# Kernel optimization log

Hardware: AMD Instinct MI355X
Metric: run time of the kernel (lower is better)

## Reference

```python
import jax, jax.numpy as jnp
import numpy as np

N = 50000      # nodes
E = 1_600_000  # edges (avg degree 32)
D = 128        # in/hidden channels
OUT = 64       # out channels


def setup_inputs() -> dict:
    key = jax.random.key(0)
    ks = jax.random.split(key, 12)
    s = 0.08  # ~glorot scale for 128-dim
    return {
        "x": jax.random.normal(ks[0], (N, D), jnp.float32),
        "edge_index": jax.random.randint(ks[1], (2, E), 0, N, dtype=jnp.int64),
        # GCN layer 1
        "W1": jax.random.normal(ks[2], (D, D), jnp.float32) * s,
        "b1": jnp.zeros((D,), jnp.float32),
        # GraphSAGE layer 2 (mean aggregation): lin_l on neighbors, lin_r on root
        "Wl": jax.random.normal(ks[3], (D, D), jnp.float32) * s,
        "Wr": jax.random.normal(ks[4], (D, D), jnp.float32) * s,
        "bs": jnp.zeros((D,), jnp.float32),
        # GAT layer 3 (heads=1, concat=False)
        "Wg": jax.random.normal(ks[5], (D, D), jnp.float32) * s,
        "a_s": jax.random.normal(ks[6], (D,), jnp.float32) * s,
        "a_d": jax.random.normal(ks[7], (D,), jnp.float32) * s,
        "bg": jnp.zeros((D,), jnp.float32),
        # GCN output layer
        "Wo": jax.random.normal(ks[8], (D, OUT), jnp.float32) * s,
        "bo": jnp.zeros((OUT,), jnp.float32),
    }


def _self_loops(src, dst, n):
    loop = jnp.arange(n, dtype=src.dtype)
    return jnp.concatenate([src, loop]), jnp.concatenate([dst, loop])


def gcn_conv(x, W, b, src, dst, n):
    # PyG GCNConv: add self-loops, symmetric normalization D^-1/2 (A+I) D^-1/2
    s2, d2 = _self_loops(src, dst, n)
    deg = jax.ops.segment_sum(jnp.ones_like(d2, dtype=x.dtype), d2, num_segments=n)
    dinv = jnp.where(deg > 0, jax.lax.rsqrt(deg), 0.0)
    h = x @ W                         # [n, out]
    norm = dinv[s2] * dinv[d2]        # [E+n]
    out = jax.ops.segment_sum(h[s2] * norm[:, None], d2, num_segments=n)
    return out + b


def sage_conv(x, Wl, Wr, b, src, dst, n):
    # PyG SAGEConv, aggr='mean': W_l * mean_neigh + W_r * x (no self-loops)
    deg = jax.ops.segment_sum(jnp.ones_like(dst, dtype=x.dtype), dst, num_segments=n)
    agg = jax.ops.segment_sum(x[src], dst, num_segments=n)
    mean = agg / jnp.maximum(deg, 1.0)[:, None]
    return mean @ Wl + x @ Wr + b


def gat_conv(x, W, a_s, a_d, b, src, dst, n):
    # PyG GATConv heads=1, concat=False: self-loops, edge softmax over incoming edges
    h = x @ W                               # [n, out]
    s2, d2 = _self_loops(src, dst, n)
    alpha_src = h @ a_s                     # [n]
    alpha_dst = h @ a_d                     # [n]
    e = jax.nn.leaky_relu(alpha_src[s2] + alpha_dst[d2], negative_slope=0.2)
    m = jax.ops.segment_max(e, d2, num_segments=n)   # every node has a self-loop
    ex = jnp.exp(e - m[d2])
    denom = jax.ops.segment_sum(ex, d2, num_segments=n)
    alpha = ex / denom[d2]
    out = jax.ops.segment_sum(alpha[:, None] * h[s2], d2, num_segments=n)
    return out + b


def reference(x, edge_index, W1, b1, Wl, Wr, bs, Wg, a_s, a_d, bg, Wo, bo):
    src, dst = edge_index[0], edge_index[1]
    n = x.shape[0]
    # eval mode: F.dropout(training=False) is identity
    h = jax.nn.relu(gcn_conv(x, W1, b1, src, dst, n))
    h = jax.nn.relu(sage_conv(h, Wl, Wr, bs, src, dst, n))
    h = jax.nn.relu(gat_conv(h, Wg, a_s, a_d, bg, src, dst, n))
    return gcn_conv(h, Wo, bo, src, dst, n)
```

## Files before the change

kernel.cpp:

```cpp
#include <hip/hip_runtime.h>
#include <math.h>


#define BUCKET_BITS 8
#define BUCKET_SZ   256
#define NBMAX       256
#define CAP         10240

typedef short short8 __attribute__((ext_vector_type(8)));
typedef float f32x4 __attribute__((ext_vector_type(4)));
typedef float f32x2 __attribute__((ext_vector_type(2)));
typedef unsigned int u32x4 __attribute__((ext_vector_type(4)));
typedef unsigned short u16x8 __attribute__((ext_vector_type(8)));
typedef int int4a __attribute__((ext_vector_type(4), aligned(4)));
typedef float float4a __attribute__((ext_vector_type(4), aligned(4)));

__device__ __forceinline__ float leaky02(float x) { return x > 0.0f ? x : 0.2f * x; }
__device__ __forceinline__ float bflo(unsigned u) { return __uint_as_float(u << 16); }
__device__ __forceinline__ float bfhi(unsigned u) { return __uint_as_float(u & 0xFFFF0000u); }
__device__ __forceinline__ unsigned short f2bf(float f) {
    unsigned u = __float_as_uint(f);
    u += 0x7FFFu + ((u >> 16) & 1u);
    return (unsigned short)(u >> 16);
}

template<int NO, bool AFP32, bool SCALE, bool BIASRELU, bool DUAL, bool DOTS>
__global__ __launch_bounds__(256) void mgemm_k(
    const void* __restrict__ Av, const float* __restrict__ W,
    const void* __restrict__ A1v, const float* __restrict__ W1,
    unsigned short* __restrict__ C16,
    const float* __restrict__ scale, const float* __restrict__ bias,
    const float* __restrict__ a_s, const float* __restrict__ a_d,
    float* __restrict__ as_, float* __restrict__ ad_, int n)
{
    constexpr int CT = NO / 16;
    __shared__ unsigned short Wp[128 * NO];
    const int tid = threadIdx.x;
    const int wave = tid >> 6, lane = tid & 63;
    const int q = lane >> 4, ml = lane & 15;
    const int row0 = blockIdx.x * 64 + wave * 16;
    int arow = row0 + ml; if (arow >= n) arow = n - 1;

    f32x4 acc[CT];
#pragma unroll
    for (int c = 0; c < CT; c++) acc[c] = {0.f, 0.f, 0.f, 0.f};

    for (int half = 0; half < (DUAL ? 2 : 1); half++) {
        const float* Wsrc = half ? W1 : W;
        const void* Asrc = half ? A1v : Av;
        __syncthreads();
        for (int f = tid; f < 64 * (NO / 4); f += 256) {
            const int kp = f / (NO / 4);
            const int n4 = f % (NO / 4);
            const float4 a = *(const float4*)(Wsrc + (size_t)(2 * kp) * NO + n4 * 4);
            const float4 b = *(const float4*)(Wsrc + (size_t)(2 * kp + 1) * NO + n4 * 4);
            const int k = 2 * kp, kb = k >> 5, qq = (k >> 3) & 3, p = (k & 7) >> 1;
            const float av[4] = {a.x, a.y, a.z, a.w};
            const float bv[4] = {b.x, b.y, b.z, b.w};
#pragma unroll
            for (int j = 0; j < 4; j++) {
                int col = n4 * 4 + j;
                int c = col >> 4, nl = col & 15;
                unsigned pk = (unsigned)f2bf(av[j]) | ((unsigned)f2bf(bv[j]) << 16);
                ((unsigned*)Wp)[(((kb * CT + c) * 64) + qq * 16 + nl) * 4 + p] = pk;
            }
        }
        __syncthreads();
#pragma unroll
        for (int kb = 0; kb < 4; kb++) {
            short8 afr;
            if (AFP32) {
                const float* Af = (const float*)Asrc + (size_t)arow * 128 + kb * 32 + q * 8;
#pragma unroll
                for (int j = 0; j < 8; j++) afr[j] = (short)f2bf(Af[j]);
            } else {
                afr = *(const short8*)((const unsigned short*)Asrc +
                                       ((size_t)kb * n + arow) * 32 + q * 8);
            }
#pragma unroll
            for (int c = 0; c < CT; c++) {
                short8 bfr = *(const short8*)(Wp + ((size_t)(kb * CT + c) * 64 + lane) * 8);
                acc[c] = __builtin_amdgcn_mfma_f32_16x16x32_bf16(afr, bfr, acc[c], 0, 0, 0);
            }
        }
    }

    if (DOTS) {
        float ps[4] = {0.f, 0.f, 0.f, 0.f}, pd[4] = {0.f, 0.f, 0.f, 0.f};
#pragma unroll
        for (int c = 0; c < CT; c++) {
            float sv = a_s[c * 16 + ml], dv = a_d[c * 16 + ml];
#pragma unroll
            for (int r = 0; r < 4; r++) {
                ps[r] = fmaf(acc[c][r], sv, ps[r]);
                pd[r] = fmaf(acc[c][r], dv, pd[r]);
            }
        }
#pragma unroll
        for (int off = 1; off < 16; off <<= 1) {
#pragma unroll
            for (int r = 0; r < 4; r++) {
                ps[r] += __shfl_xor(ps[r], off, 64);
                pd[r] += __shfl_xor(pd[r], off, 64);
            }
        }
        if (ml == 0) {
#pragma unroll
            for (int r = 0; r < 4; r++) {
                int row = row0 + q * 4 + r;
                if (row < n) { as_[row] = ps[r]; ad_[row] = pd[r]; }
            }
        }
    }

    float sc[4];
    if (SCALE) {
#pragma unroll
        for (int r = 0; r < 4; r++) {
            int row = row0 + q * 4 + r;
            sc[r] = scale[row < n ? row : 0];
        }
    }
#pragma unroll
    for (int c = 0; c < CT; c++) {
        float bv = BIASRELU ? bias[c * 16 + ml] : 0.0f;
        const int col = c * 16 + ml;
#pragma unroll
        for (int r = 0; r < 4; r++) {
            int row = row0 + q * 4 + r;
            if (row < n) {
                float v = acc[c][r];
                if (SCALE) v *= sc[r];
                if (BIASRELU) v = fmaxf(v + bv, 0.0f);
                C16[((size_t)(col >> 5) * n + row) * 32 + (col & 31)] = f2bf(v);
            }
        }
    }
}

__global__ void binit_k(int* __restrict__ bcur, int nb) {
    int t = threadIdx.x;
    if (t < nb) bcur[t] = t * CAP;
}

#define PART_CH 4096
__global__ __launch_bounds__(256) void part_k(
    const int* __restrict__ src, const int* __restrict__ dst,
    int* __restrict__ bcur, unsigned long long* __restrict__ part, int nE)
{
    __shared__ int cnt[NBMAX];
    __shared__ int cur[NBMAX];
    const int base = blockIdx.x * PART_CH;
    const int t = threadIdx.x;
    cnt[t] = 0;
    __syncthreads();
    int d[PART_CH / 256], s[PART_CH / 256];
#pragma unroll
    for (int j = 0; j < PART_CH / 256; j++) {
        int e = base + j * 256 + t;
        if (e < nE) {
            d[j] = dst[e]; s[j] = src[e];
            atomicAdd(&cnt[d[j] >> BUCKET_BITS], 1);
        } else d[j] = -1;
    }
    __syncthreads();
    {
        int c = cnt[t];
        cur[t] = c ? atomicAdd(&bcur[t], c) : 0;
    }
    __syncthreads();
#pragma unroll
    for (int j = 0; j < PART_CH / 256; j++) {
        if (d[j] >= 0) {
            int p = atomicAdd(&cur[d[j] >> BUCKET_BITS], 1);
            part[p] = ((unsigned long long)(unsigned)d[j] << 32) | (unsigned)s[j];
        }
    }
}

__global__ __launch_bounds__(256) void bscan_k(const int* __restrict__ bcur,
                                               int* __restrict__ bofs, int nb) {
    __shared__ int sm[256];
    const int t = threadIdx.x;
    int v = (t < nb) ? (bcur[t] - t * CAP) : 0;
    sm[t] = v;
    __syncthreads();
    for (int off = 1; off < 256; off <<= 1) {
        int tv = (t >= off) ? sm[t - off] : 0;
        __syncthreads();
        sm[t] += tv;
        __syncthreads();
    }
    if (t < nb) {
        bofs[t] = sm[t] - v;
        if (t == nb - 1) bofs[nb] = sm[t];
    }
}

__global__ __launch_bounds__(256) void csr_k(
    const unsigned long long* __restrict__ part, const int* __restrict__ bcur,
    const int* __restrict__ bofs, int* __restrict__ rowptr, int* __restrict__ srcs,
    float* __restrict__ dinv, float* __restrict__ invm, int n, int nE)
{
    __shared__ int lcnt[BUCKET_SZ];
    __shared__ int sm[BUCKET_SZ];
    __shared__ int lcur[BUCKET_SZ];
    const int b = blockIdx.x;
    const int t = threadIdx.x;
    const int base_in = b * CAP;
    const int cntE = bcur[b] - base_in;
    const int base_out = bofs[b];

    lcnt[t] = 0;
    __syncthreads();
#pragma unroll 4
    for (int e = t; e < cntE; e += 256) {
        int dl = (int)(part[base_in + e] >> 32) & (BUCKET_SZ - 1);
        atomicAdd(&lcnt[dl], 1);
    }
    __syncthreads();
    int v = lcnt[t];
    sm[t] = v;
    __syncthreads();
    for (int off = 1; off < 256; off <<= 1) {
        int tv = (t >= off) ? sm[t - off] : 0;
        __syncthreads();
        sm[t] += tv;
        __syncthreads();
    }
    const int excl = sm[t] - v;
    const int node = (b << BUCKET_BITS) + t;
    if (node < n) {
        rowptr[node] = base_out + excl;
        float dg = (float)v;
        dinv[node] = rsqrtf(dg + 1.0f);
        invm[node] = 1.0f / fmaxf(dg, 1.0f);
        if (node == n - 1) rowptr[n] = nE;
    }
    lcur[t] = excl;
    __syncthreads();
#pragma unroll 4
    for (int e = t; e < cntE; e += 256) {
        unsigned long long w = part[base_in + e];
        int dl = (int)(w >> 32) & (BUCKET_SZ - 1);
        int pos = atomicAdd(&lcur[dl], 1);
        srcs[base_out + pos] = (int)(unsigned)w;
    }
}

__global__ __launch_bounds__(256) void gatw_k(
    const int* __restrict__ rowptr, const int* __restrict__ srcs,
    const float* __restrict__ as_, const float* __restrict__ ad_,
    float* __restrict__ ew, float* __restrict__ rdn_, float* __restrict__ sw_, int n)
{
    const int node = blockIdx.x * 32 + (threadIdx.x >> 3);
    const int lane = threadIdx.x & 7;
    if (node >= n) return;
    const int beg = rowptr[node], end = rowptr[node + 1];
    const float ad_d = ad_[node];
    float psum = 0.f;
    for (int k = beg + lane; k < end; k += 8) {
        float e = __expf(leaky02(as_[srcs[k]] + ad_d));
        ew[k] = e;
        psum += e;
    }
#pragma unroll
    for (int off = 4; off > 0; off >>= 1) psum += __shfl_xor(psum, off, 64);
    if (lane == 0) {
        float se = __expf(leaky02(as_[node] + ad_d));
        float r = 1.0f / (psum + se);
        rdn_[node] = r;
        sw_[node] = se * r;
    }
}

template<int MODE>
__device__ __forceinline__ void edge8(
    const char* __restrict__ Hb, unsigned loff,
    const int4a ia, const int4a ib,
    const float4a wa, const float4a wb,
    f32x2* acc)
{
    const int s[8] = {ia.x, ia.y, ia.z, ia.w, ib.x, ib.y, ib.z, ib.w};
    u32x4 h[8];
#pragma unroll
    for (int j = 0; j < 8; j++)
        h[j] = *(const u32x4*)(Hb + (size_t)(((unsigned)s[j] << 6) + loff));
    const float wv[8] = {wa.x, wa.y, wa.z, wa.w, wb.x, wb.y, wb.z, wb.w};
#pragma unroll
    for (int j = 0; j < 8; j++) {
        f32x2 w2 = {wv[j], wv[j]};
#pragma unroll
        for (int c = 0; c < 4; c++) {
            f32x2 hv = {bflo(h[j][c]), bfhi(h[j][c])};
            if (MODE == 2) acc[c] = w2 * hv + acc[c];
            else           acc[c] = acc[c] + hv;
        }
    }
}

template<int NCB, int MODE>
__global__ __launch_bounds__(256, 4) void gatherbf_k(
    const unsigned short* __restrict__ H16, float* __restrict__ outf,
    unsigned short* __restrict__ out16,
    const int* __restrict__ rowptr, const int* __restrict__ srcs,
    const float* __restrict__ scl,
    const float* __restrict__ sw_,
    const float* __restrict__ ew,
    const float* __restrict__ bias, int n)
{
    constexpr int XPC = 8 / NCB;
    constexpr int NPB = 64;

    const int bid = (int)blockIdx.x;
    const int xj = bid & 7;
    const int cb = xj / XPC;
    const int NG = (n + NPB - 1) / NPB;
    const int ng = (bid >> 3) * XPC + (xj % XPC);
    if (ng >= NG) return;

    const int tid = (int)threadIdx.x;
    const int node = ng * NPB + (tid >> 2);
    if (node >= n) return;
    const int lane = tid & 3;
    const int beg = rowptr[node], end = rowptr[node + 1];
    const char* __restrict__ Hb = (const char*)H16 + (size_t)cb * n * 64;
    const unsigned loff = (unsigned)lane * 16u;

    f32x2 acc[4];
#pragma unroll
    for (int c = 0; c < 4; c++) acc[c] = {0.f, 0.f};
    const float4a wdum = {0.f, 0.f, 0.f, 0.f};

    int k = beg;
    for (; k + 16 <= end; k += 16) {
        int4a ia0 = *(const int4a*)(srcs + k);
        int4a ib0 = *(const int4a*)(srcs + k + 4);
        int4a ia1 = *(const int4a*)(srcs + k + 8);
        int4a ib1 = *(const int4a*)(srcs + k + 12);
        float4a wa0 = wdum, wb0 = wdum, wa1 = wdum, wb1 = wdum;
        if (MODE == 2) {
            wa0 = *(const float4a*)(ew + k);      wb0 = *(const float4a*)(ew + k + 4);
            wa1 = *(const float4a*)(ew + k + 8);  wb1 = *(const float4a*)(ew + k + 12);
        }
        edge8<MODE>(Hb, loff, ia0, ib0, wa0, wb0, acc);
        edge8<MODE>(Hb, loff, ia1, ib1, wa1, wb1, acc);
    }
    for (; k + 8 <= end; k += 8) {
        int4a ia = *(const int4a*)(srcs + k);
        int4a ib = *(const int4a*)(srcs + k + 4);
        float4a wa = wdum, wb = wdum;
        if (MODE == 2) {
            wa = *(const float4a*)(ew + k);  wb = *(const float4a*)(ew + k + 4);
        }
        edge8<MODE>(Hb, loff, ia, ib, wa, wb, acc);
    }
    if (k < end) {
        int4a ia = *(const int4a*)(srcs + k);
        int4a ib = *(const int4a*)(srcs + k + 4);
        int s[8] = {ia.x, ia.y, ia.z, ia.w, ib.x, ib.y, ib.z, ib.w};
        float wv[8];
        if (MODE == 2) {
            float4a wa = *(const float4a*)(ew + k);
            float4a wb = *(const float4a*)(ew + k + 4);
            wv[0] = wa.x; wv[1] = wa.y; wv[2] = wa.z; wv[3] = wa.w;
            wv[4] = wb.x; wv[5] = wb.y; wv[6] = wb.z; wv[7] = wb.w;
        }
#pragma unroll
        for (int j = 0; j < 8; j++) {
            bool act = (k + j) < end;
            s[j] = act ? s[j] : 0;
            if (MODE == 2) wv[j] = act ? wv[j] : 0.0f;
            else           wv[j] = act ? 1.0f : 0.0f;
        }
        u32x4 h[8];
#pragma unroll
        for (int j = 0; j < 8; j++)
            h[j] = *(const u32x4*)(Hb + (size_t)(((unsigned)s[j] << 6) + loff));
#pragma unroll
        for (int j = 0; j < 8; j++) {
            f32x2 w2 = {wv[j], wv[j]};
#pragma unroll
            for (int c = 0; c < 4; c++) {
                f32x2 hv = {bflo(h[j][c]), bfhi(h[j][c])};
                acc[c] = w2 * hv + acc[c];
            }
        }
    }

    const size_t orow = ((size_t)cb * n + node) * 4 + lane;
    float r[8];
    if (MODE == 0) {
        float sc = scl[node];
#pragma unroll
        for (int c = 0; c < 4; c++) { r[2*c] = acc[c].x * sc; r[2*c+1] = acc[c].y * sc; }
    } else {
        u32x4 su = *(const u32x4*)(Hb + (size_t)(((unsigned)node << 6) + loff));
        float sv[8];
#pragma unroll
        for (int c = 0; c < 4; c++) { sv[2*c] = bflo(su[c]); sv[2*c+1] = bfhi(su[c]); }
        const float4* b4 = (const float4*)bias;
        float4 ba = b4[cb * 8 + lane * 2], bb = b4[cb * 8 + lane * 2 + 1];
        float bv[8] = {ba.x, ba.y, ba.z, ba.w, bb.x, bb.y, bb.z, bb.w};
        float a8[8];
#pragma unroll
        for (int c = 0; c < 4; c++) { a8[2*c] = acc[c].x; a8[2*c+1] = acc[c].y; }
        if (MODE == 2) {
            float rden = scl[node], sw = sw_[node];
#pragma unroll
            for (int j = 0; j < 8; j++)
                r[j] = fmaxf(fmaf(rden, a8[j], fmaf(sw, sv[j], bv[j])), 0.f);
        } else {
            float dv = scl[node];
#pragma unroll
            for (int j = 0; j < 8; j++) {
                r[j] = dv * (a8[j] + sv[j]) + bv[j];
                if (MODE == 1) r[j] = fmaxf(r[j], 0.f);
            }
        }
    }
    if (MODE == 3) {
        float4* o4 = (float4*)(outf + (size_t)node * 64 + cb * 32 + lane * 8);
        float4 ra = {r[0], r[1], r[2], r[3]}, rb = {r[4], r[5], r[6], r[7]};
        o4[0] = ra; o4[1] = rb;
    } else {
        u16x8 qv;
#pragma unroll
        for (int j = 0; j < 8; j++) qv[j] = f2bf(r[j]);
        ((u16x8*)out16)[orow] = qv;
    }
}

extern "C" void kernel_launch(void* const* d_in, const int* in_sizes, int n_in,
                              void* d_out, int out_size, void* d_ws, size_t ws_size,
                              hipStream_t stream)
{
    const float* x   = (const float*)d_in[0];
    const int*   ei  = (const int*)d_in[1];
    const float* W1  = (const float*)d_in[2];
    const float* b1  = (const float*)d_in[3];
    const float* Wl  = (const float*)d_in[4];
    const float* Wr  = (const float*)d_in[5];
    const float* bs  = (const float*)d_in[6];
    const float* Wg  = (const float*)d_in[7];
    const float* a_s = (const float*)d_in[8];
    const float* a_d = (const float*)d_in[9];
    const float* bg  = (const float*)d_in[10];
    const float* Wo  = (const float*)d_in[11];
    const float* bo  = (const float*)d_in[12];

    const int n  = in_sizes[0] / 128;
    const int nE = in_sizes[1] / 2;
    const int* src = ei;
    const int* dst = ei + nE;

    char* w = (char*)d_ws;
    auto alloc = [&](size_t bytes) { char* p = w; w += (bytes + 255) & ~(size_t)255; return p; };
    unsigned short* S0 = (unsigned short*)alloc((size_t)n * 128 * 2);
    unsigned short* S1 = (unsigned short*)alloc((size_t)n * 128 * 2);
    unsigned short* S2 = (unsigned short*)alloc((size_t)n * 128 * 2);
    const int nbv = (n + BUCKET_SZ - 1) / BUCKET_SZ;
    unsigned long long* part = (unsigned long long*)alloc((size_t)nbv * CAP * 8);
    int*   srcs   = (int*)alloc((size_t)nE * 4);
    int*   rowptr = (int*)alloc((size_t)(n + 1) * 4);
    int*   bofs   = (int*)alloc((NBMAX + 1) * 4);
    int*   bcur   = (int*)alloc(NBMAX * 4);
    float* dinv   = (float*)alloc((size_t)n * 4);
    float* invm   = (float*)alloc((size_t)n * 4);
    float* as_    = (float*)alloc((size_t)n * 4);
    float* ad_    = (float*)alloc((size_t)n * 4);
    float* ew     = (float*)alloc((size_t)nE * 4);
    float* rdn_   = (float*)alloc((size_t)n * 4);
    float* sw_    = (float*)alloc((size_t)n * 4);

    const int TB = 256;
    auto cdiv = [](long long a, long long b) { return (int)((a + b - 1) / b); };
    const int nb     = nbv;
    const int gPart  = cdiv(nE, PART_CH);
    const int gGemm  = cdiv(n, 64);
    const int NG     = cdiv(n, 64);
    const int gGa128 = 8 * cdiv(NG, 2);
    const int gGa64  = 8 * cdiv(NG, 4);
    const int gGatw  = cdiv(n, 32);

    binit_k<<<1, 256, 0, stream>>>(bcur, nb);
    part_k<<<gPart, TB, 0, stream>>>(src, dst, bcur, part, nE);
    bscan_k<<<1, 256, 0, stream>>>(bcur, bofs, nb);
    csr_k<<<nb, TB, 0, stream>>>(part, bcur, bofs, rowptr, srcs, dinv, invm, n, nE);

    mgemm_k<128, true, true, false, false, false><<<gGemm, TB, 0, stream>>>(
        x, W1, nullptr, nullptr, S0, dinv, nullptr, nullptr, nullptr, nullptr, nullptr, n);
    gatherbf_k<4, 1><<<gGa128, TB, 0, stream>>>(S0, nullptr, S1, rowptr, srcs,
                                                dinv, nullptr, nullptr, b1, n);

    gatherbf_k<4, 0><<<gGa128, TB, 0, stream>>>(S1, nullptr, S0, rowptr, srcs,
                                                invm, nullptr, nullptr, nullptr, n);
    mgemm_k<128, false, false, true, true, false><<<gGemm, TB, 0, stream>>>(
        S0, Wl, S1, Wr, S2, nullptr, bs, nullptr, nullptr, nullptr, nullptr, n);

    mgemm_k<128, false, false, false, false, true><<<gGemm, TB, 0, stream>>>(
        S2, Wg, nullptr, nullptr, S1, nullptr, nullptr, a_s, a_d, as_, ad_, n);
    gatw_k<<<gGatw, TB, 0, stream>>>(rowptr, srcs, as_, ad_, ew, rdn_, sw_, n);
    gatherbf_k<4, 2><<<gGa128, TB, 0, stream>>>(S1, nullptr, S0, rowptr, srcs,
                                                rdn_, sw_, ew, bg, n);

    mgemm_k<64, false, true, false, false, false><<<gGemm, TB, 0, stream>>>(
        S0, Wo, nullptr, nullptr, S2, dinv, nullptr, nullptr, nullptr, nullptr, nullptr, n);
    gatherbf_k<2, 3><<<gGa64, TB, 0, stream>>>(S2, (float*)d_out, nullptr, rowptr, srcs,
                                               dinv, nullptr, nullptr, bo, n);
}
```

Baseline: 377.1 us.

## Renumber nodes by in-degree so gather waves process balanced rows

Adds a degree histogram, a scan and a ranking pass that permute nodes into degree-sorted order. The CSR is repacked with renumbered sources, and the whole pipeline runs in the permuted space. The first GEMM reads x through the permutation and the final gather scatters back to the original order. The aim is to balance per-wave work in the gather kernels, which it also frees from the 4-waves occupancy hint. The cost is several extra preprocessing kernels, an extra CSR copy and a serial per-node repack loop.

```diff
diff --git a/kernel.cpp b/kernel.cpp
--- a/kernel.cpp
+++ b/kernel.cpp
@@ -6,6 +6,7 @@
 #define BUCKET_SZ   256
 #define NBMAX       256
 #define CAP         10240
+#define DMAX        512
 
 typedef short short8 __attribute__((ext_vector_type(8)));
 typedef float f32x4 __attribute__((ext_vector_type(4)));
@@ -24,14 +25,15 @@
     return (unsigned short)(u >> 16);
 }
 
-template<int NO, bool AFP32, bool SCALE, bool BIASRELU, bool DUAL, bool DOTS>
+template<int NO, bool AFP32, bool SCALE, bool BIASRELU, bool DUAL, bool DOTS, bool PERM>
 __global__ __launch_bounds__(256) void mgemm_k(
     const void* __restrict__ Av, const float* __restrict__ W,
     const void* __restrict__ A1v, const float* __restrict__ W1,
     unsigned short* __restrict__ C16,
     const float* __restrict__ scale, const float* __restrict__ bias,
     const float* __restrict__ a_s, const float* __restrict__ a_d,
-    float* __restrict__ as_, float* __restrict__ ad_, int n)
+    float* __restrict__ as_, float* __restrict__ ad_,
+    const int* __restrict__ permp, int n)
 {
     constexpr int CT = NO / 16;
     __shared__ unsigned short Wp[128 * NO];
@@ -40,6 +42,7 @@
     const int q = lane >> 4, ml = lane & 15;
     const int row0 = blockIdx.x * 64 + wave * 16;
     int arow = row0 + ml; if (arow >= n) arow = n - 1;
+    const int prow = (AFP32 && PERM) ? permp[arow] : arow;
 
     f32x4 acc[CT];
 #pragma unroll
@@ -70,7 +73,7 @@
         for (int kb = 0; kb < 4; kb++) {
             short8 afr;
             if (AFP32) {
-                const float* Af = (const float*)Asrc + (size_t)arow * 128 + kb * 32 + q * 8;
+                const float* Af = (const float*)Asrc + (size_t)prow * 128 + kb * 32 + q * 8;
 #pragma unroll
                 for (int j = 0; j < 8; j++) afr[j] = (short)f2bf(Af[j]);
             } else {
@@ -138,9 +141,11 @@
     }
 }
 
-__global__ void binit_k(int* __restrict__ bcur, int nb) {
+__global__ __launch_bounds__(512) void binit_k(int* __restrict__ bcur,
+                                               int* __restrict__ ghist, int nb) {
     int t = threadIdx.x;
     if (t < nb) bcur[t] = t * CAP;
+    if (t < DMAX) ghist[t] = 0;
 }
 
 #define PART_CH 4096
@@ -200,7 +205,8 @@
 __global__ __launch_bounds__(256) void csr_k(
     const unsigned long long* __restrict__ part, const int* __restrict__ bcur,
     const int* __restrict__ bofs, int* __restrict__ rowptr, int* __restrict__ srcs,
-    float* __restrict__ dinv, float* __restrict__ invm, int n, int nE)
+    float* __restrict__ dinv, float* __restrict__ invm,
+    int* __restrict__ deg, int* __restrict__ ghist, int n, int nE)
 {
     __shared__ int lcnt[BUCKET_SZ];
     __shared__ int sm[BUCKET_SZ];
@@ -235,6 +241,8 @@
         float dg = (float)v;
         dinv[node] = rsqrtf(dg + 1.0f);
         invm[node] = 1.0f / fmaxf(dg, 1.0f);
+        deg[node] = v;
+        atomicAdd(&ghist[v < DMAX ? v : DMAX - 1], 1);
         if (node == n - 1) rowptr[n] = nE;
     }
     lcur[t] = excl;
@@ -246,6 +254,61 @@
         int pos = atomicAdd(&lcur[dl], 1);
         srcs[base_out + pos] = (int)(unsigned)w;
     }
+}
+
+__global__ __launch_bounds__(512) void dscan_k(
+    const int* __restrict__ ghist, int* __restrict__ dbase,
+    int* __restrict__ ebase, int* __restrict__ dcur)
+{
+    __shared__ int sa[DMAX], sb[DMAX];
+    const int t = threadIdx.x;
+    const int c = ghist[t];
+    sa[t] = c; sb[t] = c * t;
+    __syncthreads();
+    for (int off = 1; off < DMAX; off <<= 1) {
+        int va = (t >= off) ? sa[t - off] : 0;
+        int vb = (t >= off) ? sb[t - off] : 0;
+        __syncthreads();
+        sa[t] += va; sb[t] += vb;
+        __syncthreads();
+    }
+    dbase[t] = sa[t] - c;
+    ebase[t] = sb[t] - c * t;
+    dcur[t]  = sa[t] - c;
+}
+
+__global__ __launch_bounds__(256) void drank_k(
+    const int* __restrict__ deg, int* __restrict__ dcur,
+    const int* __restrict__ dbase, const int* __restrict__ ebase,
+    int* __restrict__ rank, int* __restrict__ perm, int* __restrict__ rowptrS,
+    const float* __restrict__ dinv, const float* __restrict__ invm,
+    float* __restrict__ dinvS, float* __restrict__ invmS, int n, int nE)
+{
+    const int node = blockIdx.x * 256 + threadIdx.x;
+    if (node >= n) return;
+    const int d = deg[node];
+    const int r = atomicAdd(&dcur[d], 1);
+    rank[node] = r;
+    perm[r] = node;
+    rowptrS[r] = ebase[d] + (r - dbase[d]) * d;
+    dinvS[r] = dinv[node];
+    invmS[r] = invm[node];
+    if (node == 0) rowptrS[n] = nE;
+}
+
+__global__ __launch_bounds__(256) void repack_k(
+    const int* __restrict__ rank, const int* __restrict__ rowptr,
+    const int* __restrict__ deg, const int* __restrict__ rowptrS,
+    const int* __restrict__ srcs, int* __restrict__ srcsS, int n)
+{
+    const int node = blockIdx.x * 256 + threadIdx.x;
+    if (node >= n) return;
+    const int r = rank[node];
+    const int ob = rowptr[node];
+    const int d = deg[node];
+    const int nb2 = rowptrS[r];
+    for (int j = 0; j < d; j++)
+        srcsS[nb2 + j] = rank[srcs[ob + j]];
 }
 
 __global__ __launch_bounds__(256) void gatw_k(
@@ -300,14 +363,16 @@
 }
 
 template<int NCB, int MODE>
-__global__ __launch_bounds__(256, 4) void gatherbf_k(
+__global__ __launch_bounds__(256) void gatherbf_k(
     const unsigned short* __restrict__ H16, float* __restrict__ outf,
     unsigned short* __restrict__ out16,
     const int* __restrict__ rowptr, const int* __restrict__ srcs,
     const float* __restrict__ scl,
     const float* __restrict__ sw_,
     const float* __restrict__ ew,
-    const float* __restrict__ bias, int n)
+    const float* __restrict__ bias,
+    const int* __restrict__ permp,
+    int n)
 {
     constexpr int XPC = 8 / NCB;
     constexpr int NPB = 64;
@@ -420,7 +485,8 @@
         }
     }
     if (MODE == 3) {
-        float4* o4 = (float4*)(outf + (size_t)node * 64 + cb * 32 + lane * 8);
+        const int pn = permp[node];
+        float4* o4 = (float4*)(outf + (size_t)pn * 64 + cb * 32 + lane * 8);
         float4 ra = {r[0], r[1], r[2], r[3]}, rb = {r[4], r[5], r[6], r[7]};
         o4[0] = ra; o4[1] = rb;
     } else {
@@ -462,50 +528,67 @@
     const int nbv = (n + BUCKET_SZ - 1) / BUCKET_SZ;
     unsigned long long* part = (unsigned long long*)alloc((size_t)nbv * CAP * 8);
     int*   srcs   = (int*)alloc((size_t)nE * 4);
+    int*   srcsS  = (int*)alloc((size_t)nE * 4);
+    float* ew     = (float*)alloc((size_t)nE * 4);
     int*   rowptr = (int*)alloc((size_t)(n + 1) * 4);
+    int*   rowptrS= (int*)alloc((size_t)(n + 1) * 4);
     int*   bofs   = (int*)alloc((NBMAX + 1) * 4);
     int*   bcur   = (int*)alloc(NBMAX * 4);
     float* dinv   = (float*)alloc((size_t)n * 4);
     float* invm   = (float*)alloc((size_t)n * 4);
+    float* dinvS  = (float*)alloc((size_t)n * 4);
+    float* invmS  = (float*)alloc((size_t)n * 4);
     float* as_    = (float*)alloc((size_t)n * 4);
     float* ad_    = (float*)alloc((size_t)n * 4);
-    float* ew     = (float*)alloc((size_t)nE * 4);
     float* rdn_   = (float*)alloc((size_t)n * 4);
     float* sw_    = (float*)alloc((size_t)n * 4);
+    int*   deg    = (int*)alloc((size_t)n * 4);
+    int*   rank   = (int*)alloc((size_t)n * 4);
+    int*   perm   = (int*)alloc((size_t)n * 4);
+    int*   ghist  = (int*)alloc(DMAX * 4);
+    int*   dbase  = (int*)alloc(DMAX * 4);
+    int*   ebase  = (int*)alloc(DMAX * 4);
+    int*   dcur   = (int*)alloc(DMAX * 4);
 
     const int TB = 256;
     auto cdiv = [](long long a, long long b) { return (int)((a + b - 1) / b); };
     const int nb     = nbv;
     const int gPart  = cdiv(nE, PART_CH);
     const int gGemm  = cdiv(n, 64);
+    const int gNode  = cdiv(n, 256);
     const int NG     = cdiv(n, 64);
     const int gGa128 = 8 * cdiv(NG, 2);
     const int gGa64  = 8 * cdiv(NG, 4);
     const int gGatw  = cdiv(n, 32);
 
-    binit_k<<<1, 256, 0, stream>>>(bcur, nb);
+    binit_k<<<1, 512, 0, stream>>>(bcur, ghist, nb);
     part_k<<<gPart, TB, 0, stream>>>(src, dst, bcur, part, nE);
     bscan_k<<<1, 256, 0, stream>>>(bcur, bofs, nb);
-    csr_k<<<nb, TB, 0, stream>>>(part, bcur, bofs, rowptr, srcs, dinv, invm, n, nE);
-
-    mgemm_k<128, true, true, false, false, false><<<gGemm, TB, 0, stream>>>(
-        x, W1, nullptr, nullptr, S0, dinv, nullptr, nullptr, nullptr, nullptr, nullptr, n);
-    gatherbf_k<4, 1><<<gGa128, TB, 0, stream>>>(S0, nullptr, S1, rowptr, srcs,
-                                                dinv, nullptr, nullptr, b1, n);
-
-    gatherbf_k<4, 0><<<gGa128, TB, 0, stream>>>(S1, nullptr, S0, rowptr, srcs,
-                                                invm, nullptr, nullptr, nullptr, n);
-    mgemm_k<128, false, false, true, true, false><<<gGemm, TB, 0, stream>>>(
-        S0, Wl, S1, Wr, S2, nullptr, bs, nullptr, nullptr, nullptr, nullptr, n);
-
-    mgemm_k<128, false, false, false, false, true><<<gGemm, TB, 0, stream>>>(
-        S2, Wg, nullptr, nullptr, S1, nullptr, nullptr, a_s, a_d, as_, ad_, n);
-    gatw_k<<<gGatw, TB, 0, stream>>>(rowptr, srcs, as_, ad_, ew, rdn_, sw_, n);
-    gatherbf_k<4, 2><<<gGa128, TB, 0, stream>>>(S1, nullptr, S0, rowptr, srcs,
-                                                rdn_, sw_, ew, bg, n);
-
-    mgemm_k<64, false, true, false, false, false><<<gGemm, TB, 0, stream>>>(
-        S0, Wo, nullptr, nullptr, S2, dinv, nullptr, nullptr, nullptr, nullptr, nullptr, n);
-    gatherbf_k<2, 3><<<gGa64, TB, 0, stream>>>(S2, (float*)d_out, nullptr, rowptr, srcs,
-                                               dinv, nullptr, nullptr, bo, n);
-}
+    csr_k<<<nb, TB, 0, stream>>>(part, bcur, bofs, rowptr, srcs, dinv, invm,
+                                 deg, ghist, n, nE);
+    dscan_k<<<1, DMAX, 0, stream>>>(ghist, dbase, ebase, dcur);
+    drank_k<<<gNode, TB, 0, stream>>>(deg, dcur, dbase, ebase, rank, perm, rowptrS,
+                                      dinv, invm, dinvS, invmS, n, nE);
+    repack_k<<<gNode, TB, 0, stream>>>(rank, rowptr, deg, rowptrS, srcs, srcsS, n);
+
+    mgemm_k<128, true, true, false, false, false, true><<<gGemm, TB, 0, stream>>>(
+        x, W1, nullptr, nullptr, S0, dinvS, nullptr, nullptr, nullptr, nullptr, nullptr, perm, n);
+    gatherbf_k<4, 1><<<gGa128, TB, 0, stream>>>(S0, nullptr, S1, rowptrS, srcsS,
+                                                dinvS, nullptr, nullptr, b1, nullptr, n);
+
+    gatherbf_k<4, 0><<<gGa128, TB, 0, stream>>>(S1, nullptr, S0, rowptrS, srcsS,
+                                                invmS, nullptr, nullptr, nullptr, nullptr, n);
+    mgemm_k<128, false, false, true, true, false, false><<<gGemm, TB, 0, stream>>>(
+        S0, Wl, S1, Wr, S2, nullptr, bs, nullptr, nullptr, nullptr, nullptr, nullptr, n);
+
+    mgemm_k<128, false, false, false, false, true, false><<<gGemm, TB, 0, stream>>>(
+        S2, Wg, nullptr, nullptr, S1, nullptr, nullptr, a_s, a_d, as_, ad_, nullptr, n);
+    gatw_k<<<gGatw, TB, 0, stream>>>(rowptrS, srcsS, as_, ad_, ew, rdn_, sw_, n);
+    gatherbf_k<4, 2><<<gGa128, TB, 0, stream>>>(S1, nullptr, S0, rowptrS, srcsS,
+                                                rdn_, sw_, ew, bg, nullptr, n);
+
+    mgemm_k<64, false, true, false, false, false, false><<<gGemm, TB, 0, stream>>>(
+        S0, Wo, nullptr, nullptr, S2, dinvS, nullptr, nullptr, nullptr, nullptr, nullptr, nullptr, n);
+    gatherbf_k<2, 3><<<gGa64, TB, 0, stream>>>(S2, (float*)d_out, nullptr, rowptrS, srcsS,
+                                               dinvS, nullptr, nullptr, bo, perm, n);
+}
```

Result: slower. 573.9 us (+52.2%).
